# Kernel tuning notes

Hardware: AMD Instinct MI355X
Metric: run time of the kernel (lower is better)

Reference implementation:

```python
import jax, jax.numpy as jnp
import numpy as np

LENGTH = 4096
BATCH = 4096
N_OBS = 2


def setup_inputs() -> dict:
    key = jax.random.key(0)
    k1, k2, k3 = jax.random.split(key, 3)
    # Scale potentials down: the original chain performs no message
    # normalization, so we keep per-step log-growth tiny to avoid overflow.
    j = jax.random.normal(k1, (), dtype=jnp.float32) * 0.01
    b = jax.random.normal(k2, (N_OBS,), dtype=jnp.float32) * 0.01
    observations = jax.random.randint(k3, (BATCH, LENGTH), 0, N_OBS, dtype=jnp.int32)
    return {"j": j, "b": b, "observations": observations}


def reference(j, b, observations):
    # Max-product belief propagation on a binary-state chain CRF,
    # vectorized over the batch and scanned over the chain length.
    B, L = observations.shape
    values = jnp.array([-0.5, 0.5], dtype=jnp.float32)          # states {0,1} - 0.5
    pairs = values[:, None] * values[None, :]                    # [2,2] outer product
    psi = jnp.exp(j * pairs)                                     # [2,2] pairwise potential
    # Unary potentials phi[b_idx, i, s] = exp(b[obs] * values[s])
    phi = jnp.exp(b[observations][..., None] * values)           # [B,L,2]
    phi_tm = jnp.transpose(phi, (1, 0, 2))                       # time-major [L,B,2]

    def step(msg, phi_t):
        # msg_new[k] = max_l phi_t[l] * msg[l] * psi[k,l]
        x = phi_t * msg                                          # [B,2]
        new = jnp.max(x[:, None, :] * psi[None, :, :], axis=2)   # [B,2]
        return new, new

    ones = jnp.ones((B, 2), dtype=phi.dtype)
    # Forward messages: column 0 is ones, column t uses obs[0..t-1]
    _, fwd_msgs = jax.lax.scan(step, ones, phi_tm[:-1])          # [L-1,B,2]
    forward = jnp.concatenate([ones[None], fwd_msgs], axis=0)    # [L,B,2]
    # Backward messages: iterate i = L-1 .. 1, last column is ones
    _, bwd_msgs = jax.lax.scan(step, ones, phi_tm[1:][::-1])     # [L-1,B,2]
    backward = jnp.concatenate([bwd_msgs[::-1], ones[None]], axis=0)  # [L,B,2]

    beliefs = phi_tm * forward * backward                        # [L,B,2]
    return jnp.transpose(beliefs, (1, 2, 0))                     # [B,2,L]
```

## Files before the change

### kernel.cpp

```cpp
#include <hip/hip_runtime.h>
#include <math.h>

#define LENGTH 4096
#define BATCH  4096
#define CHUNK  8
#define NTHR   512
#define NWAVE  (NTHR / 64)
#define ROWS   4
#define GRID   (BATCH / ROWS)

typedef float vf4 __attribute__((ext_vector_type(4)));

#define BAR() do {                                        \
    asm volatile("s_waitcnt lgkmcnt(0)" ::: "memory");    \
    __builtin_amdgcn_s_barrier();                         \
    asm volatile("" ::: "memory");                        \
  } while (0)

__device__ __forceinline__ void mp_compose(
    float a00, float a01, float a10, float a11,
    float b00, float b01, float b10, float b11,
    float& d00, float& d01, float& d10, float& d11) {
  d00 = fmaxf(a00 + b00, a01 + b10);
  d01 = fmaxf(a00 + b01, a01 + b11);
  d10 = fmaxf(a10 + b00, a11 + b10);
  d11 = fmaxf(a10 + b01, a11 + b11);
}

__device__ __forceinline__ void mp_step(
    float& f00, float& f01, float& f10, float& f11, float ui, float q) {
  float a0l0 = f00 - ui, a1l0 = f10 + ui;
  float a0l1 = f01 - ui, a1l1 = f11 + ui;
  float n00 = fmaxf(a0l0 + q, a1l0 - q);
  float n10 = fmaxf(a0l0 - q, a1l0 + q);
  float n01 = fmaxf(a0l1 + q, a1l1 - q);
  float n11 = fmaxf(a0l1 - q, a1l1 + q);
  f00 = n00; f01 = n01; f10 = n10; f11 = n11;
}

__global__ __launch_bounds__(NTHR, 8) void chain_bp_kernel(
    const float* __restrict__ jp, const float* __restrict__ bp,
    const int* __restrict__ obs, float* __restrict__ out) {
  const int tid  = threadIdx.x;
  const int lane = tid & 63;
  const int wv   = tid >> 6;

  const float LOG2E = 1.44269504088896f;
  const float j  = jp[0];
  const float q  = 0.25f * j * LOG2E;
  const float u0 = 0.5f * bp[0] * LOG2E;
  const float u1 = 0.5f * bp[1] * LOG2E;
  const float wb = -fabsf(q);

  __shared__ vf4 lut4s[16];
  __shared__ vf4 lut8[256];
  __shared__ float smp[2][NWAVE][4];
  __shared__ float sms[2][NWAVE][4];

  const int row0 = blockIdx.x * ROWS;
  const int t0   = tid * CHUNK;

  const int4* op0 = reinterpret_cast<const int4*>(obs + (size_t)row0 * LENGTH + t0);
  int4 o0 = op0[0], o1 = op0[1];

  if (tid < 16) {
    float ua = (tid & 1) ? u1 : u0;
    float f00 = -ua + q, f01 = ua - q, f10 = -ua - q, f11 = ua + q;
#pragma unroll
    for (int k = 1; k < 4; ++k)
      mp_step(f00, f01, f10, f11, ((tid >> k) & 1) ? u1 : u0, q);
    lut4s[tid] = (vf4){f00, f01, f10, f11};
  }
  BAR();
  if (tid < 256) {
    vf4 a = lut4s[tid >> 4], c = lut4s[tid & 15];
    float d00, d01, d10, d11;
    mp_compose(a[0], a[1], a[2], a[3], c[0], c[1], c[2], c[3], d00, d01, d10, d11);
    lut8[tid] = (vf4){d00, d01, d10, d11};
  }
  BAR();

#pragma unroll
  for (int r = 0; r < ROWS; ++r) {
    const int p = r & 1;

    int4 c0 = o0, c1 = o1;
    if (r + 1 < ROWS) {
      const int4* np = reinterpret_cast<const int4*>(
          obs + (size_t)(row0 + r + 1) * LENGTH + t0);
      o0 = np[0]; o1 = np[1];
    }

    float u[CHUNK];
    u[0]=c0.x?u1:u0; u[1]=c0.y?u1:u0; u[2]=c0.z?u1:u0; u[3]=c0.w?u1:u0;
    u[4]=c1.x?u1:u0; u[5]=c1.y?u1:u0; u[6]=c1.z?u1:u0; u[7]=c1.w?u1:u0;
    int idx = c0.x | (c0.y<<1) | (c0.z<<2) | (c0.w<<3)
            | (c1.x<<4) | (c1.y<<5) | (c1.z<<6) | (c1.w<<7);

    vf4 Fm = lut8[idx];
    float f00 = Fm[0], f01 = Fm[1], f10 = Fm[2], f11 = Fm[3];

    float x00 = f00, x01 = f01, x10 = f10, x11 = f11;
    float y00 = f00, y01 = f10, y10 = f01, y11 = f11;
#pragma unroll
    for (int d = 1; d < 64; d <<= 1) {
      float px00 = __shfl_up(x00, d), px01 = __shfl_up(x01, d);
      float px10 = __shfl_up(x10, d), px11 = __shfl_up(x11, d);
      float py00 = __shfl_down(y00, d), py01 = __shfl_down(y01, d);
      float py10 = __shfl_down(y10, d), py11 = __shfl_down(y11, d);
      if (lane >= d) {
        float n00, n01, n10, n11;
        mp_compose(x00, x01, x10, x11, px00, px01, px10, px11, n00, n01, n10, n11);
        x00 = n00; x01 = n01; x10 = n10; x11 = n11;
      }
      if (lane + d < 64) {
        float n00, n01, n10, n11;
        mp_compose(y00, y01, y10, y11, py00, py01, py10, py11, n00, n01, n10, n11);
        y00 = n00; y01 = n01; y10 = n10; y11 = n11;
      }
    }

    if (lane == 63) { smp[p][wv][0] = x00; smp[p][wv][1] = x01; smp[p][wv][2] = x10; smp[p][wv][3] = x11; }
    if (lane == 0)  { sms[p][wv][0] = y00; sms[p][wv][1] = y01; sms[p][wv][2] = y10; sms[p][wv][3] = y11; }
    BAR();

    float fh0 = 0.f, fh1 = 0.f;
    for (int k = 0; k < wv; ++k) {
      float m00 = smp[p][k][0], m01 = smp[p][k][1], m10 = smp[p][k][2], m11 = smp[p][k][3];
      float n0 = fmaxf(m00 + fh0, m01 + fh1);
      float n1 = fmaxf(m10 + fh0, m11 + fh1);
      fh0 = n0; fh1 = n1;
    }
    float wt0 = wb, wt1 = wb;
    for (int k = NWAVE - 1; k > wv; --k) {
      float m00 = sms[p][k][0], m01 = sms[p][k][1], m10 = sms[p][k][2], m11 = sms[p][k][3];
      float n0 = fmaxf(m00 + wt0, m01 + wt1);
      float n1 = fmaxf(m10 + wt0, m11 + wt1);
      wt0 = n0; wt1 = n1;
    }

    float z0 = fmaxf(x00 + fh0, x01 + fh1);
    float z1 = fmaxf(x10 + fh0, x11 + fh1);
    float zp0 = __shfl_up(z0, 1), zp1 = __shfl_up(z1, 1);
    float fi0 = (lane == 0) ? fh0 : zp0;
    float fi1 = (lane == 0) ? fh1 : zp1;

    float yv0 = fmaxf(y00 + wt0, y01 + wt1);
    float yv1 = fmaxf(y10 + wt0, y11 + wt1);
    float yn0 = __shfl_down(yv0, 1), yn1 = __shfl_down(yv1, 1);
    float wc0 = (lane == 63) ? wt0 : yn0;
    float wc1 = (lane == 63) ? wt1 : yn1;
    float g0 = fmaxf(q + wc0, -q + wc1);
    float g1 = fmaxf(-q + wc0, q + wc1);

    float b0[CHUNK], b1[CHUNK];
    b0[CHUNK - 1] = g0; b1[CHUNK - 1] = g1;
#pragma unroll
    for (int i = CHUNK - 1; i > 0; --i) {
      float ui = u[i];
      float a0 = b0[i] - ui;
      float a1 = b1[i] + ui;
      b0[i - 1] = fmaxf(a0 + q, a1 - q);
      b1[i - 1] = fmaxf(a0 - q, a1 + q);
    }

    float fw0 = fi0, fw1 = fi1;
    vf4 p0lo, p0hi, p1lo, p1hi;
#pragma unroll
    for (int i = 0; i < CHUNK; ++i) {
      float ui = u[i];
      float e0 = __builtin_amdgcn_exp2f(-ui + fw0 + b0[i]);
      float e1 = __builtin_amdgcn_exp2f( ui + fw1 + b1[i]);
      if (i < 4) { p0lo[i] = e0; p1lo[i] = e1; }
      else       { p0hi[i - 4] = e0; p1hi[i - 4] = e1; }
      float a0 = fw0 - ui, a1 = fw1 + ui;
      fw0 = fmaxf(a0 + q, a1 - q);
      fw1 = fmaxf(a0 - q, a1 + q);
    }
    float* outp = out + (size_t)(row0 + r) * (2 * LENGTH) + t0;
    *reinterpret_cast<vf4*>(outp)              = p0lo;
    *reinterpret_cast<vf4*>(outp + 4)          = p0hi;
    *reinterpret_cast<vf4*>(outp + LENGTH)     = p1lo;
    *reinterpret_cast<vf4*>(outp + LENGTH + 4) = p1hi;
  }
}

extern "C" void kernel_launch(void* const* d_in, const int* in_sizes, int n_in,
                              void* d_out, int out_size, void* d_ws, size_t ws_size,
                              hipStream_t stream) {
  const float* jp  = (const float*)d_in[0];
  const float* bp  = (const float*)d_in[1];
  const int*   obs = (const int*)d_in[2];
  float* out = (float*)d_out;

  chain_bp_kernel<<<GRID, NTHR, 0, stream>>>(jp, bp, obs, out);
}
```

Before: 220.6 us.

## Map one chain row per wavefront with 64-element lane chunks, removing cross-wave barrier

Result: slower. 233.1 us (+5.6%).

```diff
diff --git a/kernel.cpp b/kernel.cpp
--- a/kernel.cpp
+++ b/kernel.cpp
@@ -3,11 +3,9 @@
 
 #define LENGTH 4096
 #define BATCH  4096
-#define CHUNK  8
-#define NTHR   512
-#define NWAVE  (NTHR / 64)
-#define ROWS   4
-#define GRID   (BATCH / ROWS)
+#define NTHR   256
+#define WPB    (NTHR / 64)
+#define GRID   (BATCH / WPB)
 
 typedef float vf4 __attribute__((ext_vector_type(4)));
 
@@ -38,7 +36,7 @@
   f00 = n00; f01 = n01; f10 = n10; f11 = n11;
 }
 
-__global__ __launch_bounds__(NTHR, 8) void chain_bp_kernel(
+__global__ __launch_bounds__(NTHR, 4) void chain_bp_kernel(
     const float* __restrict__ jp, const float* __restrict__ bp,
     const int* __restrict__ obs, float* __restrict__ out) {
   const int tid  = threadIdx.x;
@@ -54,14 +52,24 @@
 
   __shared__ vf4 lut4s[16];
   __shared__ vf4 lut8[256];
-  __shared__ float smp[2][NWAVE][4];
-  __shared__ float sms[2][NWAVE][4];
 
-  const int row0 = blockIdx.x * ROWS;
-  const int t0   = tid * CHUNK;
+  const int row = blockIdx.x * WPB + wv;
+  const int t0  = lane * 64;
 
-  const int4* op0 = reinterpret_cast<const int4*>(obs + (size_t)row0 * LENGTH + t0);
-  int4 o0 = op0[0], o1 = op0[1];
+  const int4* op = reinterpret_cast<const int4*>(obs + (size_t)row * LENGTH + t0);
+  unsigned bits_lo = 0, bits_hi = 0;
+#pragma unroll
+  for (int k = 0; k < 8; ++k) {
+    int4 o = op[k];
+    unsigned nib = (o.x & 1) | ((o.y & 1) << 1) | ((o.z & 1) << 2) | ((o.w & 1) << 3);
+    bits_lo |= nib << (4 * k);
+  }
+#pragma unroll
+  for (int k = 0; k < 8; ++k) {
+    int4 o = op[8 + k];
+    unsigned nib = (o.x & 1) | ((o.y & 1) << 1) | ((o.z & 1) << 2) | ((o.w & 1) << 3);
+    bits_hi |= nib << (4 * k);
+  }
 
   if (tid < 16) {
     float ua = (tid & 1) ? u1 : u0;
@@ -72,7 +80,7 @@
     lut4s[tid] = (vf4){f00, f01, f10, f11};
   }
   BAR();
-  if (tid < 256) {
+  {
     vf4 a = lut4s[tid >> 4], c = lut4s[tid & 15];
     float d00, d01, d10, d11;
     mp_compose(a[0], a[1], a[2], a[3], c[0], c[1], c[2], c[3], d00, d01, d10, d11);
@@ -80,108 +88,94 @@
   }
   BAR();
 
+  vf4 G[8];
 #pragma unroll
-  for (int r = 0; r < ROWS; ++r) {
-    const int p = r & 1;
+  for (int s = 0; s < 4; ++s) G[s]     = lut8[(bits_lo >> (8 * s)) & 255];
+#pragma unroll
+  for (int s = 0; s < 4; ++s) G[4 + s] = lut8[(bits_hi >> (8 * s)) & 255];
 
-    int4 c0 = o0, c1 = o1;
-    if (r + 1 < ROWS) {
-      const int4* np = reinterpret_cast<const int4*>(
-          obs + (size_t)(row0 + r + 1) * LENGTH + t0);
-      o0 = np[0]; o1 = np[1];
+  float f00 = G[0][0], f01 = G[0][1], f10 = G[0][2], f11 = G[0][3];
+#pragma unroll
+  for (int s = 1; s < 8; ++s) {
+    float n00, n01, n10, n11;
+    mp_compose(G[s][0], G[s][1], G[s][2], G[s][3], f00, f01, f10, f11,
+               n00, n01, n10, n11);
+    f00 = n00; f01 = n01; f10 = n10; f11 = n11;
+  }
+
+  float x00 = f00, x01 = f01, x10 = f10, x11 = f11;
+  float y00 = f00, y01 = f10, y10 = f01, y11 = f11;
+#pragma unroll
+  for (int d = 1; d < 64; d <<= 1) {
+    float px00 = __shfl_up(x00, d), px01 = __shfl_up(x01, d);
+    float px10 = __shfl_up(x10, d), px11 = __shfl_up(x11, d);
+    float py00 = __shfl_down(y00, d), py01 = __shfl_down(y01, d);
+    float py10 = __shfl_down(y10, d), py11 = __shfl_down(y11, d);
+    if (lane >= d) {
+      float n00, n01, n10, n11;
+      mp_compose(x00, x01, x10, x11, px00, px01, px10, px11, n00, n01, n10, n11);
+      x00 = n00; x01 = n01; x10 = n10; x11 = n11;
     }
+    if (lane + d < 64) {
+      float n00, n01, n10, n11;
+      mp_compose(y00, y01, y10, y11, py00, py01, py10, py11, n00, n01, n10, n11);
+      y00 = n00; y01 = n01; y10 = n10; y11 = n11;
+    }
+  }
 
-    float u[CHUNK];
-    u[0]=c0.x?u1:u0; u[1]=c0.y?u1:u0; u[2]=c0.z?u1:u0; u[3]=c0.w?u1:u0;
-    u[4]=c1.x?u1:u0; u[5]=c1.y?u1:u0; u[6]=c1.z?u1:u0; u[7]=c1.w?u1:u0;
-    int idx = c0.x | (c0.y<<1) | (c0.z<<2) | (c0.w<<3)
-            | (c1.x<<4) | (c1.y<<5) | (c1.z<<6) | (c1.w<<7);
+  float z0 = fmaxf(x00, x01);
+  float z1 = fmaxf(x10, x11);
+  float zp0 = __shfl_up(z0, 1), zp1 = __shfl_up(z1, 1);
+  float fw0 = (lane == 0) ? 0.f : zp0;
+  float fw1 = (lane == 0) ? 0.f : zp1;
 
-    vf4 Fm = lut8[idx];
-    float f00 = Fm[0], f01 = Fm[1], f10 = Fm[2], f11 = Fm[3];
+  float yv0 = fmaxf(y00 + wb, y01 + wb);
+  float yv1 = fmaxf(y10 + wb, y11 + wb);
+  float yn0 = __shfl_down(yv0, 1), yn1 = __shfl_down(yv1, 1);
+  float wc0 = (lane == 63) ? wb : yn0;
+  float wc1 = (lane == 63) ? wb : yn1;
 
-    float x00 = f00, x01 = f01, x10 = f10, x11 = f11;
-    float y00 = f00, y01 = f10, y10 = f01, y11 = f11;
+  float wsa0[8], wsa1[8];
+  wsa0[7] = wc0; wsa1[7] = wc1;
 #pragma unroll
-    for (int d = 1; d < 64; d <<= 1) {
-      float px00 = __shfl_up(x00, d), px01 = __shfl_up(x01, d);
-      float px10 = __shfl_up(x10, d), px11 = __shfl_up(x11, d);
-      float py00 = __shfl_down(y00, d), py01 = __shfl_down(y01, d);
-      float py10 = __shfl_down(y10, d), py11 = __shfl_down(y11, d);
-      if (lane >= d) {
-        float n00, n01, n10, n11;
-        mp_compose(x00, x01, x10, x11, px00, px01, px10, px11, n00, n01, n10, n11);
-        x00 = n00; x01 = n01; x10 = n10; x11 = n11;
-      }
-      if (lane + d < 64) {
-        float n00, n01, n10, n11;
-        mp_compose(y00, y01, y10, y11, py00, py01, py10, py11, n00, n01, n10, n11);
-        y00 = n00; y01 = n01; y10 = n10; y11 = n11;
-      }
-    }
+  for (int s = 7; s > 0; --s) {
+    wsa0[s - 1] = fmaxf(G[s][0] + wsa0[s], G[s][2] + wsa1[s]);
+    wsa1[s - 1] = fmaxf(G[s][1] + wsa0[s], G[s][3] + wsa1[s]);
+  }
 
-    if (lane == 63) { smp[p][wv][0] = x00; smp[p][wv][1] = x01; smp[p][wv][2] = x10; smp[p][wv][3] = x11; }
-    if (lane == 0)  { sms[p][wv][0] = y00; sms[p][wv][1] = y01; sms[p][wv][2] = y10; sms[p][wv][3] = y11; }
-    BAR();
+  float* outp = out + (size_t)row * (2 * LENGTH) + t0;
+#pragma unroll
+  for (int s = 0; s < 8; ++s) {
+    unsigned byte = ((s < 4) ? (bits_lo >> (8 * s)) : (bits_hi >> (8 * (s - 4)))) & 255;
+    float us[8];
+#pragma unroll
+    for (int i = 0; i < 8; ++i) us[i] = ((byte >> i) & 1) ? u1 : u0;
 
-    float fh0 = 0.f, fh1 = 0.f;
-    for (int k = 0; k < wv; ++k) {
-      float m00 = smp[p][k][0], m01 = smp[p][k][1], m10 = smp[p][k][2], m11 = smp[p][k][3];
-      float n0 = fmaxf(m00 + fh0, m01 + fh1);
-      float n1 = fmaxf(m10 + fh0, m11 + fh1);
-      fh0 = n0; fh1 = n1;
-    }
-    float wt0 = wb, wt1 = wb;
-    for (int k = NWAVE - 1; k > wv; --k) {
-      float m00 = sms[p][k][0], m01 = sms[p][k][1], m10 = sms[p][k][2], m11 = sms[p][k][3];
-      float n0 = fmaxf(m00 + wt0, m01 + wt1);
-      float n1 = fmaxf(m10 + wt0, m11 + wt1);
-      wt0 = n0; wt1 = n1;
-    }
-
-    float z0 = fmaxf(x00 + fh0, x01 + fh1);
-    float z1 = fmaxf(x10 + fh0, x11 + fh1);
-    float zp0 = __shfl_up(z0, 1), zp1 = __shfl_up(z1, 1);
-    float fi0 = (lane == 0) ? fh0 : zp0;
-    float fi1 = (lane == 0) ? fh1 : zp1;
-
-    float yv0 = fmaxf(y00 + wt0, y01 + wt1);
-    float yv1 = fmaxf(y10 + wt0, y11 + wt1);
-    float yn0 = __shfl_down(yv0, 1), yn1 = __shfl_down(yv1, 1);
-    float wc0 = (lane == 63) ? wt0 : yn0;
-    float wc1 = (lane == 63) ? wt1 : yn1;
-    float g0 = fmaxf(q + wc0, -q + wc1);
-    float g1 = fmaxf(-q + wc0, q + wc1);
-
-    float b0[CHUNK], b1[CHUNK];
-    b0[CHUNK - 1] = g0; b1[CHUNK - 1] = g1;
+    float b0[8], b1[8];
+    b0[7] = fmaxf( q + wsa0[s], -q + wsa1[s]);
+    b1[7] = fmaxf(-q + wsa0[s],  q + wsa1[s]);
 #pragma unroll
-    for (int i = CHUNK - 1; i > 0; --i) {
-      float ui = u[i];
-      float a0 = b0[i] - ui;
-      float a1 = b1[i] + ui;
+    for (int i = 7; i > 0; --i) {
+      float a0 = b0[i] - us[i], a1 = b1[i] + us[i];
       b0[i - 1] = fmaxf(a0 + q, a1 - q);
       b1[i - 1] = fmaxf(a0 - q, a1 + q);
     }
 
-    float fw0 = fi0, fw1 = fi1;
     vf4 p0lo, p0hi, p1lo, p1hi;
 #pragma unroll
-    for (int i = 0; i < CHUNK; ++i) {
-      float ui = u[i];
-      float e0 = __builtin_amdgcn_exp2f(-ui + fw0 + b0[i]);
-      float e1 = __builtin_amdgcn_exp2f( ui + fw1 + b1[i]);
+    for (int i = 0; i < 8; ++i) {
+      float e0 = __builtin_amdgcn_exp2f(-us[i] + fw0 + b0[i]);
+      float e1 = __builtin_amdgcn_exp2f( us[i] + fw1 + b1[i]);
       if (i < 4) { p0lo[i] = e0; p1lo[i] = e1; }
       else       { p0hi[i - 4] = e0; p1hi[i - 4] = e1; }
-      float a0 = fw0 - ui, a1 = fw1 + ui;
+      float a0 = fw0 - us[i], a1 = fw1 + us[i];
       fw0 = fmaxf(a0 + q, a1 - q);
       fw1 = fmaxf(a0 - q, a1 + q);
     }
-    float* outp = out + (size_t)(row0 + r) * (2 * LENGTH) + t0;
-    *reinterpret_cast<vf4*>(outp)              = p0lo;
-    *reinterpret_cast<vf4*>(outp + 4)          = p0hi;
-    *reinterpret_cast<vf4*>(outp + LENGTH)     = p1lo;
-    *reinterpret_cast<vf4*>(outp + LENGTH + 4) = p1hi;
+    *reinterpret_cast<vf4*>(outp + 8 * s)              = p0lo;
+    *reinterpret_cast<vf4*>(outp + 8 * s + 4)          = p0hi;
+    *reinterpret_cast<vf4*>(outp + LENGTH + 8 * s)     = p1lo;
+    *reinterpret_cast<vf4*>(outp + LENGTH + 8 * s + 4) = p1hi;
   }
 }
 
```

## Process two rows per block with interleaved wave scans and one barrier

Applied to the files above, without the earlier changes.

New measurement: 222.3 us. No clear change (+0.8%).

```diff
diff --git a/kernel.cpp b/kernel.cpp
--- a/kernel.cpp
+++ b/kernel.cpp
@@ -6,8 +6,8 @@
 #define CHUNK  8
 #define NTHR   512
 #define NWAVE  (NTHR / 64)
-#define ROWS   4
-#define GRID   (BATCH / ROWS)
+#define RPB    2
+#define GRID   (BATCH / RPB)
 
 typedef float vf4 __attribute__((ext_vector_type(4)));
 
@@ -38,6 +38,71 @@
   f00 = n00; f01 = n01; f10 = n10; f11 = n11;
 }
 
+__device__ __forceinline__ void row_epilogue(
+    float x00, float x01, float x10, float x11,
+    float y00, float y01, float y10, float y11,
+    int idx, const float (*smpR)[4], const float (*smsR)[4],
+    float* __restrict__ outp, int wv, int lane,
+    float q, float u0, float u1, float wb) {
+  float fh0 = 0.f, fh1 = 0.f;
+  for (int k = 0; k < wv; ++k) {
+    float m00 = smpR[k][0], m01 = smpR[k][1], m10 = smpR[k][2], m11 = smpR[k][3];
+    float n0 = fmaxf(m00 + fh0, m01 + fh1);
+    float n1 = fmaxf(m10 + fh0, m11 + fh1);
+    fh0 = n0; fh1 = n1;
+  }
+  float wt0 = wb, wt1 = wb;
+  for (int k = NWAVE - 1; k > wv; --k) {
+    float m00 = smsR[k][0], m01 = smsR[k][1], m10 = smsR[k][2], m11 = smsR[k][3];
+    float n0 = fmaxf(m00 + wt0, m01 + wt1);
+    float n1 = fmaxf(m10 + wt0, m11 + wt1);
+    wt0 = n0; wt1 = n1;
+  }
+
+  float z0 = fmaxf(x00 + fh0, x01 + fh1);
+  float z1 = fmaxf(x10 + fh0, x11 + fh1);
+  float zp0 = __shfl_up(z0, 1), zp1 = __shfl_up(z1, 1);
+  float fw0 = (lane == 0) ? fh0 : zp0;
+  float fw1 = (lane == 0) ? fh1 : zp1;
+
+  float yv0 = fmaxf(y00 + wt0, y01 + wt1);
+  float yv1 = fmaxf(y10 + wt0, y11 + wt1);
+  float yn0 = __shfl_down(yv0, 1), yn1 = __shfl_down(yv1, 1);
+  float wc0 = (lane == 63) ? wt0 : yn0;
+  float wc1 = (lane == 63) ? wt1 : yn1;
+  float g0 = fmaxf(q + wc0, -q + wc1);
+  float g1 = fmaxf(-q + wc0, q + wc1);
+
+  float u[CHUNK];
+#pragma unroll
+  for (int i = 0; i < CHUNK; ++i) u[i] = ((idx >> i) & 1) ? u1 : u0;
+
+  float b0[CHUNK], b1[CHUNK];
+  b0[CHUNK - 1] = g0; b1[CHUNK - 1] = g1;
+#pragma unroll
+  for (int i = CHUNK - 1; i > 0; --i) {
+    float a0 = b0[i] - u[i], a1 = b1[i] + u[i];
+    b0[i - 1] = fmaxf(a0 + q, a1 - q);
+    b1[i - 1] = fmaxf(a0 - q, a1 + q);
+  }
+
+  vf4 p0lo, p0hi, p1lo, p1hi;
+#pragma unroll
+  for (int i = 0; i < CHUNK; ++i) {
+    float e0 = __builtin_amdgcn_exp2f(-u[i] + fw0 + b0[i]);
+    float e1 = __builtin_amdgcn_exp2f( u[i] + fw1 + b1[i]);
+    if (i < 4) { p0lo[i] = e0; p1lo[i] = e1; }
+    else       { p0hi[i - 4] = e0; p1hi[i - 4] = e1; }
+    float a0 = fw0 - u[i], a1 = fw1 + u[i];
+    fw0 = fmaxf(a0 + q, a1 - q);
+    fw1 = fmaxf(a0 - q, a1 + q);
+  }
+  *reinterpret_cast<vf4*>(outp)              = p0lo;
+  *reinterpret_cast<vf4*>(outp + 4)          = p0hi;
+  *reinterpret_cast<vf4*>(outp + LENGTH)     = p1lo;
+  *reinterpret_cast<vf4*>(outp + LENGTH + 4) = p1hi;
+}
+
 __global__ __launch_bounds__(NTHR, 8) void chain_bp_kernel(
     const float* __restrict__ jp, const float* __restrict__ bp,
     const int* __restrict__ obs, float* __restrict__ out) {
@@ -54,14 +119,16 @@
 
   __shared__ vf4 lut4s[16];
   __shared__ vf4 lut8[256];
-  __shared__ float smp[2][NWAVE][4];
-  __shared__ float sms[2][NWAVE][4];
-
-  const int row0 = blockIdx.x * ROWS;
+  __shared__ float smp[RPB][NWAVE][4];
+  __shared__ float sms[RPB][NWAVE][4];
+
+  const int rowA = blockIdx.x * RPB;
   const int t0   = tid * CHUNK;
 
-  const int4* op0 = reinterpret_cast<const int4*>(obs + (size_t)row0 * LENGTH + t0);
-  int4 o0 = op0[0], o1 = op0[1];
+  const int4* pA = reinterpret_cast<const int4*>(obs + (size_t)rowA * LENGTH + t0);
+  const int4* pB = reinterpret_cast<const int4*>(obs + (size_t)(rowA + 1) * LENGTH + t0);
+  int4 a0 = pA[0], a1 = pA[1];
+  int4 c0 = pB[0], c1 = pB[1];
 
   if (tid < 16) {
     float ua = (tid & 1) ? u1 : u0;
@@ -80,109 +147,59 @@
   }
   BAR();
 
-#pragma unroll
-  for (int r = 0; r < ROWS; ++r) {
-    const int p = r & 1;
-
-    int4 c0 = o0, c1 = o1;
-    if (r + 1 < ROWS) {
-      const int4* np = reinterpret_cast<const int4*>(
-          obs + (size_t)(row0 + r + 1) * LENGTH + t0);
-      o0 = np[0]; o1 = np[1];
+  int idxA = a0.x | (a0.y<<1) | (a0.z<<2) | (a0.w<<3)
+           | (a1.x<<4) | (a1.y<<5) | (a1.z<<6) | (a1.w<<7);
+  int idxB = c0.x | (c0.y<<1) | (c0.z<<2) | (c0.w<<3)
+           | (c1.x<<4) | (c1.y<<5) | (c1.z<<6) | (c1.w<<7);
+  vf4 FA = lut8[idxA];
+  vf4 FB = lut8[idxB];
+
+  float xA00 = FA[0], xA01 = FA[1], xA10 = FA[2], xA11 = FA[3];
+  float yA00 = FA[0], yA01 = FA[2], yA10 = FA[1], yA11 = FA[3];
+  float xB00 = FB[0], xB01 = FB[1], xB10 = FB[2], xB11 = FB[3];
+  float yB00 = FB[0], yB01 = FB[2], yB10 = FB[1], yB11 = FB[3];
+#pragma unroll
+  for (int d = 1; d < 64; d <<= 1) {
+    float pA00 = __shfl_up(xA00, d), pA01 = __shfl_up(xA01, d);
+    float pA10 = __shfl_up(xA10, d), pA11 = __shfl_up(xA11, d);
+    float qA00 = __shfl_down(yA00, d), qA01 = __shfl_down(yA01, d);
+    float qA10 = __shfl_down(yA10, d), qA11 = __shfl_down(yA11, d);
+    float pB00 = __shfl_up(xB00, d), pB01 = __shfl_up(xB01, d);
+    float pB10 = __shfl_up(xB10, d), pB11 = __shfl_up(xB11, d);
+    float qB00 = __shfl_down(yB00, d), qB01 = __shfl_down(yB01, d);
+    float qB10 = __shfl_down(yB10, d), qB11 = __shfl_down(yB11, d);
+    if (lane >= d) {
+      float n00, n01, n10, n11;
+      mp_compose(xA00, xA01, xA10, xA11, pA00, pA01, pA10, pA11, n00, n01, n10, n11);
+      xA00 = n00; xA01 = n01; xA10 = n10; xA11 = n11;
+      mp_compose(xB00, xB01, xB10, xB11, pB00, pB01, pB10, pB11, n00, n01, n10, n11);
+      xB00 = n00; xB01 = n01; xB10 = n10; xB11 = n11;
     }
-
-    float u[CHUNK];
-    u[0]=c0.x?u1:u0; u[1]=c0.y?u1:u0; u[2]=c0.z?u1:u0; u[3]=c0.w?u1:u0;
-    u[4]=c1.x?u1:u0; u[5]=c1.y?u1:u0; u[6]=c1.z?u1:u0; u[7]=c1.w?u1:u0;
-    int idx = c0.x | (c0.y<<1) | (c0.z<<2) | (c0.w<<3)
-            | (c1.x<<4) | (c1.y<<5) | (c1.z<<6) | (c1.w<<7);
-
-    vf4 Fm = lut8[idx];
-    float f00 = Fm[0], f01 = Fm[1], f10 = Fm[2], f11 = Fm[3];
-
-    float x00 = f00, x01 = f01, x10 = f10, x11 = f11;
-    float y00 = f00, y01 = f10, y10 = f01, y11 = f11;
-#pragma unroll
-    for (int d = 1; d < 64; d <<= 1) {
-      float px00 = __shfl_up(x00, d), px01 = __shfl_up(x01, d);
-      float px10 = __shfl_up(x10, d), px11 = __shfl_up(x11, d);
-      float py00 = __shfl_down(y00, d), py01 = __shfl_down(y01, d);
-      float py10 = __shfl_down(y10, d), py11 = __shfl_down(y11, d);
-      if (lane >= d) {
-        float n00, n01, n10, n11;
-        mp_compose(x00, x01, x10, x11, px00, px01, px10, px11, n00, n01, n10, n11);
-        x00 = n00; x01 = n01; x10 = n10; x11 = n11;
-      }
-      if (lane + d < 64) {
-        float n00, n01, n10, n11;
-        mp_compose(y00, y01, y10, y11, py00, py01, py10, py11, n00, n01, n10, n11);
-        y00 = n00; y01 = n01; y10 = n10; y11 = n11;
-      }
+    if (lane + d < 64) {
+      float n00, n01, n10, n11;
+      mp_compose(yA00, yA01, yA10, yA11, qA00, qA01, qA10, qA11, n00, n01, n10, n11);
+      yA00 = n00; yA01 = n01; yA10 = n10; yA11 = n11;
+      mp_compose(yB00, yB01, yB10, yB11, qB00, qB01, qB10, qB11, n00, n01, n10, n11);
+      yB00 = n00; yB01 = n01; yB10 = n10; yB11 = n11;
     }
-
-    if (lane == 63) { smp[p][wv][0] = x00; smp[p][wv][1] = x01; smp[p][wv][2] = x10; smp[p][wv][3] = x11; }
-    if (lane == 0)  { sms[p][wv][0] = y00; sms[p][wv][1] = y01; sms[p][wv][2] = y10; sms[p][wv][3] = y11; }
-    BAR();
-
-    float fh0 = 0.f, fh1 = 0.f;
-    for (int k = 0; k < wv; ++k) {
-      float m00 = smp[p][k][0], m01 = smp[p][k][1], m10 = smp[p][k][2], m11 = smp[p][k][3];
-      float n0 = fmaxf(m00 + fh0, m01 + fh1);
-      float n1 = fmaxf(m10 + fh0, m11 + fh1);
-      fh0 = n0; fh1 = n1;
-    }
-    float wt0 = wb, wt1 = wb;
-    for (int k = NWAVE - 1; k > wv; --k) {
-      float m00 = sms[p][k][0], m01 = sms[p][k][1], m10 = sms[p][k][2], m11 = sms[p][k][3];
-      float n0 = fmaxf(m00 + wt0, m01 + wt1);
-      float n1 = fmaxf(m10 + wt0, m11 + wt1);
-      wt0 = n0; wt1 = n1;
-    }
-
-    float z0 = fmaxf(x00 + fh0, x01 + fh1);
-    float z1 = fmaxf(x10 + fh0, x11 + fh1);
-    float zp0 = __shfl_up(z0, 1), zp1 = __shfl_up(z1, 1);
-    float fi0 = (lane == 0) ? fh0 : zp0;
-    float fi1 = (lane == 0) ? fh1 : zp1;
-
-    float yv0 = fmaxf(y00 + wt0, y01 + wt1);
-    float yv1 = fmaxf(y10 + wt0, y11 + wt1);
-    float yn0 = __shfl_down(yv0, 1), yn1 = __shfl_down(yv1, 1);
-    float wc0 = (lane == 63) ? wt0 : yn0;
-    float wc1 = (lane == 63) ? wt1 : yn1;
-    float g0 = fmaxf(q + wc0, -q + wc1);
-    float g1 = fmaxf(-q + wc0, q + wc1);
-
-    float b0[CHUNK], b1[CHUNK];
-    b0[CHUNK - 1] = g0; b1[CHUNK - 1] = g1;
-#pragma unroll
-    for (int i = CHUNK - 1; i > 0; --i) {
-      float ui = u[i];
-      float a0 = b0[i] - ui;
-      float a1 = b1[i] + ui;
-      b0[i - 1] = fmaxf(a0 + q, a1 - q);
-      b1[i - 1] = fmaxf(a0 - q, a1 + q);
-    }
-
-    float fw0 = fi0, fw1 = fi1;
-    vf4 p0lo, p0hi, p1lo, p1hi;
-#pragma unroll
-    for (int i = 0; i < CHUNK; ++i) {
-      float ui = u[i];
-      float e0 = __builtin_amdgcn_exp2f(-ui + fw0 + b0[i]);
-      float e1 = __builtin_amdgcn_exp2f( ui + fw1 + b1[i]);
-      if (i < 4) { p0lo[i] = e0; p1lo[i] = e1; }
-      else       { p0hi[i - 4] = e0; p1hi[i - 4] = e1; }
-      float a0 = fw0 - ui, a1 = fw1 + ui;
-      fw0 = fmaxf(a0 + q, a1 - q);
-      fw1 = fmaxf(a0 - q, a1 + q);
-    }
-    float* outp = out + (size_t)(row0 + r) * (2 * LENGTH) + t0;
-    *reinterpret_cast<vf4*>(outp)              = p0lo;
-    *reinterpret_cast<vf4*>(outp + 4)          = p0hi;
-    *reinterpret_cast<vf4*>(outp + LENGTH)     = p1lo;
-    *reinterpret_cast<vf4*>(outp + LENGTH + 4) = p1hi;
-  }
+  }
+
+  if (lane == 63) {
+    smp[0][wv][0] = xA00; smp[0][wv][1] = xA01; smp[0][wv][2] = xA10; smp[0][wv][3] = xA11;
+    smp[1][wv][0] = xB00; smp[1][wv][1] = xB01; smp[1][wv][2] = xB10; smp[1][wv][3] = xB11;
+  }
+  if (lane == 0) {
+    sms[0][wv][0] = yA00; sms[0][wv][1] = yA01; sms[0][wv][2] = yA10; sms[0][wv][3] = yA11;
+    sms[1][wv][0] = yB00; sms[1][wv][1] = yB01; sms[1][wv][2] = yB10; sms[1][wv][3] = yB11;
+  }
+  BAR();
+
+  float* outA = out + (size_t)rowA * (2 * LENGTH) + t0;
+  row_epilogue(xA00, xA01, xA10, xA11, yA00, yA01, yA10, yA11,
+               idxA, smp[0], sms[0], outA, wv, lane, q, u0, u1, wb);
+  float* outB = out + (size_t)(rowA + 1) * (2 * LENGTH) + t0;
+  row_epilogue(xB00, xB01, xB10, xB11, yB00, yB01, yB10, yB11,
+               idxB, smp[1], sms[1], outB, wv, lane, q, u0, u1, wb);
 }
 
 extern "C" void kernel_launch(void* const* d_in, const int* in_sizes, int n_in,
```
